# Kernel tuning notes

Measured on AMD Instinct MI355X. Metric: run time of the kernel, lower is better.

## Reference

```python
import jax, jax.numpy as jnp
import numpy as np

N_EMBD = 384
HEAD_SIZE = 64
B, T = 16, 2048


def setup_inputs() -> dict:
    key = jax.random.key(0)
    ks = jax.random.split(key, 7)
    s = 1.0 / np.sqrt(N_EMBD)
    return {
        "x": jax.random.normal(ks[0], (B, T, N_EMBD), dtype=jnp.float32),
        "Wq": jax.random.uniform(ks[1], (N_EMBD, HEAD_SIZE), jnp.float32, -s, s),
        "bq": jax.random.uniform(ks[2], (HEAD_SIZE,), jnp.float32, -s, s),
        "Wk": jax.random.uniform(ks[3], (N_EMBD, HEAD_SIZE), jnp.float32, -s, s),
        "bk": jax.random.uniform(ks[4], (HEAD_SIZE,), jnp.float32, -s, s),
        "Wv": jax.random.uniform(ks[5], (N_EMBD, HEAD_SIZE), jnp.float32, -s, s),
        "bv": jax.random.uniform(ks[6], (HEAD_SIZE,), jnp.float32, -s, s),
    }


def reference(x, Wq, bq, Wk, bk, Wv, bv):
    # QKV projections: [B,T,C] @ [C,H] -> [B,T,H]
    q = x @ Wq + bq
    k = x @ Wk + bk
    v = x @ Wv + bv
    scale = k.shape[-1] ** (-0.5)
    # NOTE: original forward applies NO causal mask (tril buffer unused).
    scores = jnp.einsum("bqh,bkh->bqk", q, k) * scale  # [B,T,T]
    wmap = jax.nn.softmax(scores, axis=-1)
    # dropout is identity in eval mode
    out = jnp.einsum("bqk,bkh->bqh", wmap, v)  # [B,T,H]
    return out
```

## Files before the change

### kernel.cpp

```cpp
#include <hip/hip_runtime.h>
#include <hip/hip_bf16.h>
#include <cstdint>

typedef unsigned short u16;
typedef __attribute__((ext_vector_type(8))) short short8;
typedef __attribute__((ext_vector_type(4))) short short4v;
typedef __attribute__((ext_vector_type(4))) float f32x4;

#define MFMA16(a, b, c) __builtin_amdgcn_mfma_f32_16x16x32_bf16((a), (b), (c), 0, 0, 0)

constexpr int Bn   = 16;
constexpr int Tn   = 2048;
constexpr int Cn   = 384;
constexpr int Hn   = 64;
constexpr long NTOK = (long)Bn * Tn;
constexpr long NELT = NTOK * Hn;
constexpr int SPLITS = 2;

#define QSCALE 0.18033688011112042f

__device__ __forceinline__ u16 f2bf(float f) {
  union { float f; uint32_t u; } c; c.f = f;
  uint32_t u = c.u;
  return (u16)((u + 0x7fffu + ((u >> 16) & 1u)) >> 16);
}

__device__ __forceinline__ uint32_t pkbf(float a, float b) {
  uint32_t d;
  asm("v_cvt_pk_bf16_f32 %0, %1, %2" : "=v"(d) : "v"(a), "v"(b));
  return d;
}

__device__ __forceinline__ short8 ldx8(const float* p) {
  const float4 f0 = *reinterpret_cast<const float4*>(p);
  const float4 f1 = *reinterpret_cast<const float4*>(p + 4);
  union { short8 s8; uint32_t u[4]; } r;
  r.u[0] = pkbf(f0.x, f0.y); r.u[1] = pkbf(f0.z, f0.w);
  r.u[2] = pkbf(f1.x, f1.y); r.u[3] = pkbf(f1.z, f1.w);
  return r.s8;
}

__device__ __forceinline__ void gl16(const u16* g, const u16* l) {
  __builtin_amdgcn_global_load_lds(
      (const __attribute__((address_space(1))) void*)g,
      (__attribute__((address_space(3))) void*)l, 16, 0, 0);
}

__global__ __launch_bounds__(256) void wtrans(
    const float* __restrict__ Wq, const float* __restrict__ Wk,
    const float* __restrict__ Wv, u16* __restrict__ wtd)
{
  __shared__ u16 tile[64][65];
  const int m  = blockIdx.x / 6;
  const int kc = blockIdx.x % 6;
  const float* W = (m == 0) ? Wq : (m == 1) ? Wk : Wv;
  const int t = threadIdx.x;

  {
    const int kr = t >> 2, seg = t & 3;
    const float* src = W + (size_t)(kc * 64 + kr) * Hn + seg * 16;
    #pragma unroll
    for (int j = 0; j < 4; ++j) {
      const float4 f = *reinterpret_cast<const float4*>(src + j * 4);
      u16* p = &tile[kr][seg * 16 + j * 4];
      p[0] = f2bf(f.x); p[1] = f2bf(f.y); p[2] = f2bf(f.z); p[3] = f2bf(f.w);
    }
  }
  __syncthreads();
  {
    const int hr = t >> 2, seg = t & 3;
    union { short8 s; u16 u[8]; } o0, o1;
    #pragma unroll
    for (int j = 0; j < 8; ++j) o0.u[j] = tile[seg * 16 + j][hr];
    #pragma unroll
    for (int j = 0; j < 8; ++j) o1.u[j] = tile[seg * 16 + 8 + j][hr];
    u16* dst = wtd + ((size_t)m * 64 + hr) * Cn + kc * 64 + seg * 16;
    *reinterpret_cast<short8*>(dst)     = o0.s;
    *reinterpret_cast<short8*>(dst + 8) = o1.s;
  }
}

__global__ __launch_bounds__(256, 2) void qkv_proj(
    const float* __restrict__ x, const u16* __restrict__ wtd,
    const float* __restrict__ bq, const float* __restrict__ bk,
    const float* __restrict__ bv,
    u16* __restrict__ oq, u16* __restrict__ ok, u16* __restrict__ ovt)
{
  __shared__ u16 wbuf[3][3 * 64 * 64];

  const int t    = threadIdx.x;
  const int lane = t & 63;
  const int w    = t >> 6;
  const int l15  = lane & 15;
  const int lh   = lane >> 4;
  const long r0  = (long)blockIdx.x * 64;

  int srcoff[6];
  #pragma unroll
  for (int i = 0; i < 6; ++i) {
    const int g = i * 256 + t;
    const int r = g >> 3, c = g & 7;
    srcoff[i] = r * Cn + ((c ^ (r & 7)) << 3);
  }
  const int ldsb = w * 64 * 8;

  const float* xrow = x + (r0 + w * 16 + l15) * Cn;

  const int cks0 = ((lh)     ^ (l15 & 7)) << 3;
  const int cks1 = ((lh + 4) ^ (l15 & 7)) << 3;

  f32x4 acc[3][4];
  #pragma unroll
  for (int m = 0; m < 3; ++m)
    #pragma unroll
    for (int n = 0; n < 4; ++n) acc[m][n] = f32x4{0.f, 0.f, 0.f, 0.f};

  #pragma unroll
  for (int i = 0; i < 6; ++i)
    gl16(wtd + srcoff[i], &wbuf[0][(i * 256) * 8 + ldsb]);
  short8 aCur0 = ldx8(xrow + lh * 8);
  short8 aCur1 = ldx8(xrow + 32 + lh * 8);
  #pragma unroll
  for (int i = 0; i < 6; ++i)
    gl16(wtd + 64 + srcoff[i], &wbuf[1][(i * 256) * 8 + ldsb]);
  short8 aNx10 = ldx8(xrow + 64 + lh * 8);
  short8 aNx11 = ldx8(xrow + 96 + lh * 8);
  short8 aNx20, aNx21;
  asm volatile("s_waitcnt vmcnt(14)" ::: "memory");
  __builtin_amdgcn_s_barrier();
  __builtin_amdgcn_sched_barrier(0);

  for (int kc = 0; kc < 6; ++kc) {
    const int cb = kc % 3;
    const int sb = (kc + 2) % 3;
    if (kc + 2 < 6) {
      #pragma unroll
      for (int i = 0; i < 6; ++i)
        gl16(wtd + (kc + 2) * 64 + srcoff[i], &wbuf[sb][(i * 256) * 8 + ldsb]);
      const float* p = xrow + (kc + 2) * 64 + lh * 8;
      aNx20 = ldx8(p);
      aNx21 = ldx8(p + 32);
    }

    const u16* wc = &wbuf[cb][0];
    #pragma unroll
    for (int m = 0; m < 3; ++m)
      #pragma unroll
      for (int n = 0; n < 4; ++n) {
        const int row = m * 64 + n * 16 + l15;
        const short8 b0 = *reinterpret_cast<const short8*>(&wc[row * 64 + cks0]);
        acc[m][n] = MFMA16(aCur0, b0, acc[m][n]);
        const short8 b1 = *reinterpret_cast<const short8*>(&wc[row * 64 + cks1]);
        acc[m][n] = MFMA16(aCur1, b1, acc[m][n]);
      }

    if (kc + 1 < 6) {
      if (kc + 2 < 6) asm volatile("s_waitcnt vmcnt(14)" ::: "memory");
      else            asm volatile("s_waitcnt vmcnt(4)"  ::: "memory");
      __builtin_amdgcn_s_barrier();
      __builtin_amdgcn_sched_barrier(0);
      aCur0 = aNx10; aCur1 = aNx11;
      aNx10 = aNx20; aNx11 = aNx21;
    }
  }

  {
    const float* bias[2] = {bq, bk};
    u16*         dst[2]  = {oq, ok};
    const float  scl[2]  = {QSCALE, 1.0f};
    #pragma unroll
    for (int m = 0; m < 2; ++m) {
      #pragma unroll
      for (int n = 0; n < 4; ++n) {
        int col = n * 16 + l15;
        float bb = bias[m][col];
        #pragma unroll
        for (int r = 0; r < 4; ++r) {
          int row = lh * 4 + r;
          dst[m][(r0 + w * 16 + row) * Hn + col] = f2bf((acc[m][n][r] + bb) * scl[m]);
        }
      }
    }
  }
  {
    const long g    = r0 + w * 16 + lh * 4;
    const long bidx = g >> 11;
    const long tloc = g & 2047;
    const int  u    = (int)(tloc & 63);
    const long tb   = tloc & ~63L;
    const int  slotb = 32 * ((u >> 5) & 1) + 8 * ((u >> 2) & 3) + 4 * ((u >> 4) & 1);
    #pragma unroll
    for (int n = 0; n < 4; ++n) {
      int col = n * 16 + l15;
      float bb = bv[col];
      short4v pk;
      #pragma unroll
      for (int r = 0; r < 4; ++r) pk[r] = (short)f2bf(acc[2][n][r] + bb);
      *reinterpret_cast<short4v*>(ovt + (bidx * Hn + col) * Tn + tb + slotb) = pk;
    }
  }
}

__global__ __launch_bounds__(256, 2) void flash_attn(
    const u16* __restrict__ q, const u16* __restrict__ k,
    const u16* __restrict__ vt, u16* __restrict__ opart,
    float* __restrict__ lpart)
{
  __shared__ u16 kbuf[4][64 * 64];
  __shared__ u16 vbuf[4][64 * 64];

  const int t    = threadIdx.x;
  const int lane = t & 63;
  const int w    = t >> 6;
  const int l15  = lane & 15;
  const int lh   = lane >> 4;
  const int swz_id = (blockIdx.x & 7) * 64 + (blockIdx.x >> 3);
  const int b     = swz_id / 32;
  const int rem   = swz_id % 32;
  const int split = rem / 16;
  const int qt    = rem % 16;
  const long rowbase = (long)b * Tn + qt * 128;
  const int it0 = split * 16;

  short8 aq[2][2];
  #pragma unroll
  for (int qg = 0; qg < 2; ++qg) {
    const u16* qrow = q + (rowbase + w * 32 + qg * 16 + l15) * Hn;
    aq[qg][0] = *reinterpret_cast<const short8*>(qrow + lh * 8);
    aq[qg][1] = *reinterpret_cast<const short8*>(qrow + 32 + lh * 8);
  }

  union { short8 s8; uint32_t u[4]; } ON;
  #pragma unroll
  for (int i = 0; i < 4; ++i) ON.u[i] = 0x3F803F80u;

  f32x4 o[2][4];
  #pragma unroll
  for (int qg = 0; qg < 2; ++qg)
    #pragma unroll
    for (int m = 0; m < 4; ++m) o[qg][m] = f32x4{0.f, 0.f, 0.f, 0.f};
  f32x4 ls0 = f32x4{0.f, 0.f, 0.f, 0.f};
  f32x4 ls1 = f32x4{0.f, 0.f, 0.f, 0.f};

  const u16* kb_g = k  + (long)b * Tn * Hn;
  const u16* vb_g = vt + (long)b * Hn * Tn;

  const int g0 = t, g1 = 256 + t;
  const int r0g = g0 >> 3, c0g = g0 & 7;
  const int r1g = g1 >> 3, c1g = g1 & 7;
  const long ksrc0 = (long)r0g * Hn + ((c0g ^ (r0g & 7)) << 3);
  const long ksrc1 = (long)r1g * Hn + ((c1g ^ (r1g & 7)) << 3);
  const long vsrc0 = (long)r0g * Tn + ((c0g ^ (r0g & 7)) << 3);
  const long vsrc1 = (long)r1g * Tn + ((c1g ^ (r1g & 7)) << 3);
  const int wb0 = w * 64 * 8;
  const int wb1 = wb0 + 256 * 8;

  const int swz  = l15 & 7;
  const int cks0 = ((0 * 4 + lh) ^ swz) << 3;
  const int cks1 = ((1 * 4 + lh) ^ swz) << 3;
  const int rfr  = l15 * 64;

  auto stage = [&](int it, int bs) {
    const u16* kt = kb_g + (long)it * 64 * Hn;
    const u16* vp = vb_g + it * 64;
    gl16(kt + ksrc0, &kbuf[bs][wb0]);
    gl16(kt + ksrc1, &kbuf[bs][wb1]);
    gl16(vp + vsrc0, &vbuf[bs][wb0]);
    gl16(vp + vsrc1, &vbuf[bs][wb1]);
  };

  auto tile_compute = [&](int bs) {
    const u16* kc  = &kbuf[bs][0];
    const u16* vcb = &vbuf[bs][0];

    f32x4 s0[4], s1[4];
    #pragma unroll
    for (int n = 0; n < 4; ++n) { s0[n] = f32x4{0.f,0.f,0.f,0.f}; s1[n] = f32x4{0.f,0.f,0.f,0.f}; }
    __builtin_amdgcn_s_setprio(1);
    #pragma unroll
    for (int n = 0; n < 4; ++n) {
      const short8 ak0 = *reinterpret_cast<const short8*>(&kc[n * 1024 + rfr + cks0]);
      const short8 ak1 = *reinterpret_cast<const short8*>(&kc[n * 1024 + rfr + cks1]);
      s0[n] = MFMA16(ak0, aq[0][0], s0[n]);
      s0[n] = MFMA16(ak1, aq[0][1], s0[n]);
      s1[n] = MFMA16(ak0, aq[1][0], s1[n]);
      s1[n] = MFMA16(ak1, aq[1][1], s1[n]);
    }
    __builtin_amdgcn_s_setprio(0);

    #pragma unroll
    for (int n = 0; n < 4; ++n)
      #pragma unroll
      for (int r = 0; r < 4; ++r) {
        s0[n][r] = __builtin_amdgcn_exp2f(s0[n][r]);
        s1[n][r] = __builtin_amdgcn_exp2f(s1[n][r]);
      }

    union { short8 s8; uint32_t u[4]; } B00, B01, B10, B11;
    B00.u[0] = pkbf(s0[0][0], s0[0][1]); B00.u[1] = pkbf(s0[0][2], s0[0][3]);
    B00.u[2] = pkbf(s0[1][0], s0[1][1]); B00.u[3] = pkbf(s0[1][2], s0[1][3]);
    B01.u[0] = pkbf(s0[2][0], s0[2][1]); B01.u[1] = pkbf(s0[2][2], s0[2][3]);
    B01.u[2] = pkbf(s0[3][0], s0[3][1]); B01.u[3] = pkbf(s0[3][2], s0[3][3]);
    B10.u[0] = pkbf(s1[0][0], s1[0][1]); B10.u[1] = pkbf(s1[0][2], s1[0][3]);
    B10.u[2] = pkbf(s1[1][0], s1[1][1]); B10.u[3] = pkbf(s1[1][2], s1[1][3]);
    B11.u[0] = pkbf(s1[2][0], s1[2][1]); B11.u[1] = pkbf(s1[2][2], s1[2][3]);
    B11.u[2] = pkbf(s1[3][0], s1[3][1]); B11.u[3] = pkbf(s1[3][2], s1[3][3]);

    __builtin_amdgcn_s_setprio(1);
    #pragma unroll
    for (int m = 0; m < 4; ++m) {
      const short8 av0 = *reinterpret_cast<const short8*>(&vcb[m * 1024 + rfr + cks0]);
      const short8 av1 = *reinterpret_cast<const short8*>(&vcb[m * 1024 + rfr + cks1]);
      o[0][m] = MFMA16(av0, B00.s8, o[0][m]);
      o[0][m] = MFMA16(av1, B01.s8, o[0][m]);
      o[1][m] = MFMA16(av0, B10.s8, o[1][m]);
      o[1][m] = MFMA16(av1, B11.s8, o[1][m]);
    }
    ls0 = MFMA16(ON.s8, B00.s8, ls0);
    ls0 = MFMA16(ON.s8, B01.s8, ls0);
    ls1 = MFMA16(ON.s8, B10.s8, ls1);
    ls1 = MFMA16(ON.s8, B11.s8, ls1);
    __builtin_amdgcn_s_setprio(0);
  };

  stage(it0 + 0, 0);
  stage(it0 + 1, 1);
  stage(it0 + 2, 2);
  stage(it0 + 3, 3);
  asm volatile("s_waitcnt vmcnt(8)" ::: "memory");
  __builtin_amdgcn_s_barrier();
  __builtin_amdgcn_sched_barrier(0);

  for (int p = 0; p < 8; ++p) {
    const int bA = (2 * p) & 3;
    const int bB = (2 * p + 1) & 3;
    tile_compute(bA);
    tile_compute(bB);

    if (p < 7) {
      asm volatile("s_waitcnt vmcnt(0)" ::: "memory");
      __builtin_amdgcn_s_barrier();
      __builtin_amdgcn_sched_barrier(0);
      if (p < 6) {
        stage(it0 + 2 * p + 4, bA);
        stage(it0 + 2 * p + 5, bB);
      }
    }
  }

  #pragma unroll
  for (int qg = 0; qg < 2; ++qg) {
    const float tot = (qg == 0) ? ls0[0] : ls1[0];
    const long qrow = rowbase + w * 32 + qg * 16 + l15;
    u16* od = opart + ((long)split * NELT) + qrow * Hn;
    #pragma unroll
    for (int m = 0; m < 4; ++m) {
      uint32_t p0 = pkbf(o[qg][m][0], o[qg][m][1]);
      uint32_t p1 = pkbf(o[qg][m][2], o[qg][m][3]);
      uint32_t* dst = reinterpret_cast<uint32_t*>(od + m * 16 + lh * 4);
      dst[0] = p0; dst[1] = p1;
    }
    if (lh == 0) lpart[(long)split * NTOK + qrow] = tot;
  }
}

__global__ __launch_bounds__(256) void combine(
    const u16* __restrict__ op, const float* __restrict__ lp,
    float* __restrict__ out)
{
  const long idx  = (long)blockIdx.x * 256 + threadIdx.x;
  const long base = idx * 8;
  const long row  = base >> 6;
  float lsum = 0.f;
  #pragma unroll
  for (int s = 0; s < SPLITS; ++s) lsum += lp[s * NTOK + row];
  const float linv = 1.0f / lsum;

  float acc[8] = {0.f, 0.f, 0.f, 0.f, 0.f, 0.f, 0.f, 0.f};
  #pragma unroll
  for (int s = 0; s < SPLITS; ++s) {
    union { short8 v; u16 u[8]; } pk;
    pk.v = *reinterpret_cast<const short8*>(op + s * NELT + base);
    #pragma unroll
    for (int j = 0; j < 8; ++j) {
      union { uint32_t u; float f; } c; c.u = ((uint32_t)pk.u[j]) << 16;
      acc[j] += c.f;
    }
  }
  float4 r0, r1;
  r0.x = acc[0] * linv; r0.y = acc[1] * linv; r0.z = acc[2] * linv; r0.w = acc[3] * linv;
  r1.x = acc[4] * linv; r1.y = acc[5] * linv; r1.z = acc[6] * linv; r1.w = acc[7] * linv;
  *reinterpret_cast<float4*>(out + base)     = r0;
  *reinterpret_cast<float4*>(out + base + 4) = r1;
}

extern "C" void kernel_launch(void* const* d_in, const int* in_sizes, int n_in,
                              void* d_out, int out_size, void* d_ws, size_t ws_size,
                              hipStream_t stream) {
  const float* x  = (const float*)d_in[0];
  const float* Wq = (const float*)d_in[1];
  const float* bq = (const float*)d_in[2];
  const float* Wk = (const float*)d_in[3];
  const float* bk = (const float*)d_in[4];
  const float* Wv = (const float*)d_in[5];
  const float* bv = (const float*)d_in[6];
  float* out = (float*)d_out;

  u16* qs  = (u16*)d_ws;
  u16* ks  = qs + NELT;
  u16* vs  = ks + NELT;
  u16* wtd = vs + NELT;
  u16* op  = wtd + 3 * 64 * Cn;
  float* lp = (float*)(op + (long)SPLITS * NELT);

  hipLaunchKernelGGL(wtrans, dim3(18), dim3(256), 0, stream, Wq, Wk, Wv, wtd);
  hipLaunchKernelGGL(qkv_proj, dim3((int)(NTOK / 64)), dim3(256), 0, stream,
                     x, wtd, bq, bk, bv, qs, ks, vs);
  hipLaunchKernelGGL(flash_attn, dim3(16 * 16 * SPLITS), dim3(256), 0, stream,
                     qs, ks, vs, op, lp);
  hipLaunchKernelGGL(combine, dim3((int)(NELT / 8 / 256)), dim3(256), 0, stream,
                     op, lp, out);
}
```

Baseline: 50.17 us.

## Remove split-K in flash attention and drop the combine kernel

Each flash-attention block now processes the full key range (32 tiles) instead of half, so the grid shrinks from 512 to 256 blocks. The output is normalized in-kernel and written directly as fp32. This removes the combine launch and the bf16 partial-output round trip through global memory. In exchange, parallelism is halved: 256 blocks may underfill the 256 CUs at two blocks per CU, and per-block latency doubles.

```diff
diff --git a/kernel.cpp b/kernel.cpp
--- a/kernel.cpp
+++ b/kernel.cpp
@@ -15,7 +15,6 @@
 constexpr int Hn   = 64;
 constexpr long NTOK = (long)Bn * Tn;
 constexpr long NELT = NTOK * Hn;
-constexpr int SPLITS = 2;
 
 #define QSCALE 0.18033688011112042f
 
@@ -203,8 +202,7 @@
 
 __global__ __launch_bounds__(256, 2) void flash_attn(
     const u16* __restrict__ q, const u16* __restrict__ k,
-    const u16* __restrict__ vt, u16* __restrict__ opart,
-    float* __restrict__ lpart)
+    const u16* __restrict__ vt, float* __restrict__ out)
 {
   __shared__ u16 kbuf[4][64 * 64];
   __shared__ u16 vbuf[4][64 * 64];
@@ -214,13 +212,10 @@
   const int w    = t >> 6;
   const int l15  = lane & 15;
   const int lh   = lane >> 4;
-  const int swz_id = (blockIdx.x & 7) * 64 + (blockIdx.x >> 3);
-  const int b     = swz_id / 32;
-  const int rem   = swz_id % 32;
-  const int split = rem / 16;
-  const int qt    = rem % 16;
+  const int swz_id = (blockIdx.x & 7) * 32 + (blockIdx.x >> 3);
+  const int b     = swz_id / 16;
+  const int qt    = swz_id % 16;
   const long rowbase = (long)b * Tn + qt * 128;
-  const int it0 = split * 16;
 
   short8 aq[2][2];
   #pragma unroll
@@ -323,75 +318,44 @@
     __builtin_amdgcn_s_setprio(0);
   };
 
-  stage(it0 + 0, 0);
-  stage(it0 + 1, 1);
-  stage(it0 + 2, 2);
-  stage(it0 + 3, 3);
+  stage(0, 0);
+  stage(1, 1);
+  stage(2, 2);
+  stage(3, 3);
   asm volatile("s_waitcnt vmcnt(8)" ::: "memory");
   __builtin_amdgcn_s_barrier();
   __builtin_amdgcn_sched_barrier(0);
 
-  for (int p = 0; p < 8; ++p) {
+  for (int p = 0; p < 16; ++p) {
     const int bA = (2 * p) & 3;
     const int bB = (2 * p + 1) & 3;
     tile_compute(bA);
     tile_compute(bB);
 
-    if (p < 7) {
+    if (p < 15) {
       asm volatile("s_waitcnt vmcnt(0)" ::: "memory");
       __builtin_amdgcn_s_barrier();
       __builtin_amdgcn_sched_barrier(0);
-      if (p < 6) {
-        stage(it0 + 2 * p + 4, bA);
-        stage(it0 + 2 * p + 5, bB);
+      if (p < 14) {
+        stage(2 * p + 4, bA);
+        stage(2 * p + 5, bB);
       }
     }
   }
 
   #pragma unroll
   for (int qg = 0; qg < 2; ++qg) {
-    const float tot = (qg == 0) ? ls0[0] : ls1[0];
+    const float inv = 1.0f / ((qg == 0) ? ls0[0] : ls1[0]);
     const long qrow = rowbase + w * 32 + qg * 16 + l15;
-    u16* od = opart + ((long)split * NELT) + qrow * Hn;
+    float* od = out + qrow * Hn;
     #pragma unroll
     for (int m = 0; m < 4; ++m) {
-      uint32_t p0 = pkbf(o[qg][m][0], o[qg][m][1]);
-      uint32_t p1 = pkbf(o[qg][m][2], o[qg][m][3]);
-      uint32_t* dst = reinterpret_cast<uint32_t*>(od + m * 16 + lh * 4);
-      dst[0] = p0; dst[1] = p1;
-    }
-    if (lh == 0) lpart[(long)split * NTOK + qrow] = tot;
-  }
-}
-
-__global__ __launch_bounds__(256) void combine(
-    const u16* __restrict__ op, const float* __restrict__ lp,
-    float* __restrict__ out)
-{
-  const long idx  = (long)blockIdx.x * 256 + threadIdx.x;
-  const long base = idx * 8;
-  const long row  = base >> 6;
-  float lsum = 0.f;
-  #pragma unroll
-  for (int s = 0; s < SPLITS; ++s) lsum += lp[s * NTOK + row];
-  const float linv = 1.0f / lsum;
-
-  float acc[8] = {0.f, 0.f, 0.f, 0.f, 0.f, 0.f, 0.f, 0.f};
-  #pragma unroll
-  for (int s = 0; s < SPLITS; ++s) {
-    union { short8 v; u16 u[8]; } pk;
-    pk.v = *reinterpret_cast<const short8*>(op + s * NELT + base);
-    #pragma unroll
-    for (int j = 0; j < 8; ++j) {
-      union { uint32_t u; float f; } c; c.u = ((uint32_t)pk.u[j]) << 16;
-      acc[j] += c.f;
-    }
-  }
-  float4 r0, r1;
-  r0.x = acc[0] * linv; r0.y = acc[1] * linv; r0.z = acc[2] * linv; r0.w = acc[3] * linv;
-  r1.x = acc[4] * linv; r1.y = acc[5] * linv; r1.z = acc[6] * linv; r1.w = acc[7] * linv;
-  *reinterpret_cast<float4*>(out + base)     = r0;
-  *reinterpret_cast<float4*>(out + base + 4) = r1;
+      float4 vv;
+      vv.x = o[qg][m][0] * inv; vv.y = o[qg][m][1] * inv;
+      vv.z = o[qg][m][2] * inv; vv.w = o[qg][m][3] * inv;
+      *reinterpret_cast<float4*>(od + m * 16 + lh * 4) = vv;
+    }
+  }
 }
 
 extern "C" void kernel_launch(void* const* d_in, const int* in_sizes, int n_in,
@@ -410,14 +374,10 @@
   u16* ks  = qs + NELT;
   u16* vs  = ks + NELT;
   u16* wtd = vs + NELT;
-  u16* op  = wtd + 3 * 64 * Cn;
-  float* lp = (float*)(op + (long)SPLITS * NELT);
 
   hipLaunchKernelGGL(wtrans, dim3(18), dim3(256), 0, stream, Wq, Wk, Wv, wtd);
   hipLaunchKernelGGL(qkv_proj, dim3((int)(NTOK / 64)), dim3(256), 0, stream,
                      x, wtd, bq, bk, bv, qs, ks, vs);
-  hipLaunchKernelGGL(flash_attn, dim3(16 * 16 * SPLITS), dim3(256), 0, stream,
-                     qs, ks, vs, op, lp);
-  hipLaunchKernelGGL(combine, dim3((int)(NELT / 8 / 256)), dim3(256), 0, stream,
-                     op, lp, out);
-}
+  hipLaunchKernelGGL(flash_attn, dim3(256), dim3(256), 0, stream,
+                     qs, ks, vs, out);
+}
```

Result: slower. 52.91 us (+5.5%).
